# Optimization experiments

Hardware: AMD Instinct MI355X
Metric: run time of the kernel (lower is better)

Reference implementation:

```python
import jax, jax.numpy as jnp
import numpy as np

N_MAX = 5000  # original module truncates both clouds to 5000 points


def _hungarian(cost):
    """Exact linear sum assignment (Jonker-Volgenant / Hungarian with potentials).
    cost: (n, n) float64 numpy array. Returns cols: cols[i] = column assigned to row i.
    Matches scipy.optimize.linear_sum_assignment on square matrices."""
    n = cost.shape[0]
    u = np.zeros(n + 1)
    v = np.zeros(n + 1)
    p = np.full(n + 1, -1, dtype=np.int64)  # p[j] = row matched to column j (-1 = free); col n is virtual
    way = np.zeros(n, dtype=np.int64)
    for i in range(n):
        p[n] = i
        j0 = n
        minv = np.full(n, np.inf)
        used = np.zeros(n + 1, dtype=bool)
        # Dijkstra-style shortest augmenting path, inner step vectorized over columns
        while p[j0] != -1:
            used[j0] = True
            i0 = p[j0]
            free = ~used[:n]
            cur = cost[i0] - u[i0] - v[:n]
            upd = free & (cur < minv)
            minv = np.where(upd, cur, minv)
            way = np.where(upd, j0, way)
            masked = np.where(free, minv, np.inf)
            j1 = int(np.argmin(masked))
            delta = masked[j1]
            used_idx = np.nonzero(used)[0]
            u[p[used_idx]] += delta
            v[used_idx] -= delta
            minv = np.where(free, minv - delta, minv)
            j0 = j1
        # augment along alternating path back to the virtual column
        while j0 != n:
            j1 = way[j0]
            p[j0] = p[j1]
            j0 = int(j1)
    cols = np.empty(n, dtype=np.int64)
    cols[p[:n]] = np.arange(n)
    return cols


def _pairwise_dist(a, b):
    # Euclidean cdist: (n,3) x (m,3) -> (n,m)
    d2 = (jnp.sum(a * a, axis=1)[:, None]
          + jnp.sum(b * b, axis=1)[None, :]
          - 2.0 * (a @ b.T))
    return jnp.sqrt(jnp.maximum(d2, 0.0))


def setup_inputs() -> dict:
    key = jax.random.key(0)
    k1, k2 = jax.random.split(key)
    gt_pc = jax.random.normal(k1, (1, 1024, 3), dtype=jnp.float32)
    gen_pc = jax.random.normal(k2, (1, 1024, 3), dtype=jnp.float32)
    return {"gt_pc": gt_pc, "gen_pc": gen_pc}


def reference(gt_pc, gen_pc):
    # squeeze() + truncate to 5000 points, as in the torch module
    a = gt_pc.reshape(-1, gt_pc.shape[-1])[:N_MAX]
    b = gen_pc.reshape(-1, gen_pc.shape[-1])[:N_MAX]
    d = _pairwise_dist(a, b)  # (n, n) full cost matrix
    # exact optimal assignment (host-side, data dependent -> not jittable)
    cols = _hungarian(np.asarray(d, dtype=np.float64))
    rows = jnp.arange(d.shape[0])
    return d[rows, jnp.asarray(cols)].mean()
```

## Files before the change

kernel.cpp:

```cpp
#include <hip/hip_runtime.h>
#include <math.h>


#define N         1024
#define NT        512
#define NW        (NT / 64)
#define CPL       16
#define NPHASE    3
#define ROUND_CAP 30000

typedef unsigned long long ull;

__device__ __forceinline__ float wave_min_bcast(float x) {
#define DPPSTEP(C) { int _t = __builtin_amdgcn_update_dpp(                    \
      __float_as_int(x), __float_as_int(x), (C), 0xf, 0xf, false);            \
      x = fminf(x, __int_as_float(_t)); }
    DPPSTEP(0x111)
    DPPSTEP(0x112)
    DPPSTEP(0x114)
    DPPSTEP(0x118)
    DPPSTEP(0x142)
    DPPSTEP(0x143)
#undef DPPSTEP
    return __int_as_float(__builtin_amdgcn_readlane(__float_as_int(x), 63));
}

__device__ __forceinline__ float dist_b(const float4 Ai, float bxn, float byn,
                                        float bzn, float sbk) {
    float acc = fmaf(bzn, Ai.z, sbk);
    acc = fmaf(byn, Ai.y, acc);
    acc = fmaf(bxn, Ai.x, acc);
    return __builtin_amdgcn_sqrtf(fmaxf(acc + Ai.w, 0.0f));
}

__global__ __launch_bounds__(NT, 1)
void emd_auction(const float* __restrict__ gt, const float* __restrict__ gen,
                 float* __restrict__ out)
{
    __shared__ float4 A[N];
    __shared__ float4 B[N];
    __shared__ float  p[N];
    __shared__ ull    bidPack[N];
    __shared__ int    owner[N];
    __shared__ int    pobj[N];
    __shared__ int    freeBuf[2][N];
    __shared__ int    bidList[N];
    __shared__ int    bidFlag[N];
    __shared__ int    s_cnt[2];
    __shared__ int    s_nbid;
    __shared__ double partial[NW];

    const int tid  = threadIdx.x;
    const int lane = tid & 63;
    const int wid  = tid >> 6;

    float bxn[CPL], byn[CPL], bzn[CPL], sb[CPL];
    #pragma unroll
    for (int k = 0; k < CPL; ++k) {
        const int j = (k << 6) | lane;
        const float gx = gen[3*j], gy = gen[3*j+1], gz = gen[3*j+2];
        bxn[k] = -2.f*gx; byn[k] = -2.f*gy; bzn[k] = -2.f*gz;
        sb[k]  = gx*gx + gy*gy + gz*gz;
    }
    for (int i = tid; i < N; i += NT) {
        const float x = gt[3*i], y = gt[3*i+1], z = gt[3*i+2];
        A[i] = make_float4(x, y, z, x*x + y*y + z*z);
        const float gx = gen[3*i], gy = gen[3*i+1], gz = gen[3*i+2];
        B[i] = make_float4(gx, gy, gz, gx*gx + gy*gy + gz*gz);
        p[i] = 0.f; bidPack[i] = 0ull; bidFlag[i] = 0;
        owner[i] = -1; pobj[i] = -1;
    }
    if (tid == 0) s_nbid = 0;
    __syncthreads();

    const float EPS[NPHASE] = {0.25f, 0.033f, 4e-3f};
    int  rounds  = 0;
    bool aborted = false;
    int  cur     = 0;

    for (int ph = 0; ph < NPHASE && !aborted; ++ph) {
        const float eps = EPS[ph];

        if (ph > 0) {
            for (int i = wid; i < N; i += NW) {
                const int j = pobj[i];
                if (j < 0) continue;
                const float4 Ai = A[i];
                float m1 = INFINITY;
                #pragma unroll
                for (int k = 0; k < CPL; ++k) {
                    const int jj = (k << 6) | lane;
                    m1 = fminf(m1, dist_b(Ai, bxn[k], byn[k], bzn[k], sb[k])
                                   + p[jj]);
                }
                const float g1 = wave_min_bcast(m1);
                const float4 Bj = B[j];
                const float dot = Ai.x*Bj.x + Ai.y*Bj.y + Ai.z*Bj.z;
                const float rcj = __builtin_amdgcn_sqrtf(
                                      fmaxf(Ai.w + Bj.w - 2.f*dot, 0.f)) + p[j];
                if (rcj > g1 + eps && lane == 0) { owner[j] = -1; pobj[i] = -1; }
            }
            __syncthreads();
        }
        if (tid == 0) { s_cnt[0] = 0; s_cnt[1] = 0; }
        cur = 0;
        __syncthreads();
        for (int base = 0; base < N; base += NT) {
            const int i = base + tid;
            const bool fr = (pobj[i] < 0);
            const ull m = __ballot(fr);
            int pos = 0;
            if (lane == 0 && m) pos = atomicAdd(&s_cnt[0], __popcll(m));
            pos = __shfl(pos, 0);
            if (fr) freeBuf[0][pos + __popcll(m & ((1ull << lane) - 1ull))] = i;
        }
        __syncthreads();

        for (;;) {
            const int nf = s_cnt[cur];
            if (nf == 0) break;
            if (++rounds >= ROUND_CAP) { aborted = true; break; }
            const int nxt = cur ^ 1;
            if (tid == 0) s_cnt[nxt] = 0;

            for (int t = wid; t < nf; t += NW) {
                const int i = freeBuf[cur][t];
                const float4 Ai = A[i];
                float m1 = INFINITY, m2 = INFINITY; int a1 = 0;
                #pragma unroll
                for (int k = 0; k < CPL; ++k) {
                    const int j = (k << 6) | lane;
                    const float rc =
                        dist_b(Ai, bxn[k], byn[k], bzn[k], sb[k]) + p[j];
                    if (rc < m1)      { m2 = m1; m1 = rc; a1 = j; }
                    else if (rc < m2) { m2 = rc; }
                }
                const float g1 = wave_min_bcast(m1);
                const ull  mm  = __ballot(m1 == g1);
                const int  w1  = __ffsll(mm) - 1;
                const int  j1  = __builtin_amdgcn_readlane(a1, w1);
                const float contrib = (lane == w1) ? m2 : m1;
                const float g2 = wave_min_bcast(contrib);
                if (lane == 0) {
                    const float bid = p[j1] + (g2 - g1) + eps;
                    atomicMax(&bidPack[j1],
                              ((ull)(unsigned)__float_as_int(bid) << 32)
                              | (unsigned)i);
                    if (atomicCAS(&bidFlag[j1], 0, 1) == 0) {
                        const int pos = atomicAdd(&s_nbid, 1);
                        bidList[pos] = j1;
                    }
                }
            }
            __syncthreads();

            const int nbid = s_nbid;
            for (int t = tid; t < nbid; t += NT) {
                const int j  = bidList[t];
                const ull pk = bidPack[j];
                bidPack[j] = 0ull; bidFlag[j] = 0;
                p[j] = __int_as_float((int)(pk >> 32));
                const int inew = (int)(pk & 0xffffffffu);
                const int iold = owner[j];
                owner[j] = inew;
                pobj[inew] = j;
                if (iold >= 0) {
                    pobj[iold] = -1;
                    const int pos = atomicAdd(&s_cnt[nxt], 1);
                    freeBuf[nxt][pos] = iold;
                }
            }
            __syncthreads();

            if (tid == 0) s_nbid = 0;
            for (int base = 0; base < nf; base += NT) {
                const int t = base + tid;
                bool fr = false; int i = 0;
                if (t < nf) { i = freeBuf[cur][t]; fr = (pobj[i] < 0); }
                const ull m = __ballot(fr);
                int pos = 0;
                if (lane == 0 && m) pos = atomicAdd(&s_cnt[nxt], __popcll(m));
                pos = __shfl(pos, 0);
                if (fr)
                    freeBuf[nxt][pos + __popcll(m & ((1ull << lane) - 1ull))] = i;
            }
            __syncthreads();
            cur = nxt;
        }
    }

    {
        const int leftover = s_cnt[cur];
        if (leftover > 0) {
            if (wid == 0) {
                for (int t = 0; t < leftover; ++t) {
                    const int i = freeBuf[cur][t];
                    const float4 Ai = A[i];
                    float m1 = INFINITY; int a1 = 0;
                    #pragma unroll
                    for (int k = 0; k < CPL; ++k) {
                        const int j = (k << 6) | lane;
                        const bool fre = (owner[j] < 0);
                        const float c = dist_b(Ai, bxn[k], byn[k], bzn[k], sb[k]);
                        const float sel = fre ? c : INFINITY;
                        if (sel < m1) { m1 = sel; a1 = j; }
                    }
                    const float g1 = wave_min_bcast(m1);
                    const ull  mm  = __ballot(m1 == g1);
                    const int  w1  = __ffsll(mm) - 1;
                    const int  j1  = __builtin_amdgcn_readlane(a1, w1);
                    if (lane == 0) owner[j1] = i;
                    asm volatile("s_waitcnt lgkmcnt(0)" ::: "memory");
                }
            }
            __syncthreads();
        }
    }

    double s = 0.0;
    for (int j = tid; j < N; j += NT) {
        const int i = owner[j];
        if (i >= 0) {
            const float4 Ai = A[i];
            const float4 Bj = B[j];
            const float dot = Ai.x*Bj.x + Ai.y*Bj.y + Ai.z*Bj.z;
            const float d2  = Ai.w + Bj.w - 2.0f*dot;
            s += (double)__builtin_amdgcn_sqrtf(fmaxf(d2, 0.0f));
        }
    }
    #pragma unroll
    for (int m = 32; m >= 1; m >>= 1) s += __shfl_xor(s, m);
    if (lane == 0) partial[wid] = s;
    __syncthreads();
    if (tid == 0) {
        double tot = 0.0;
        for (int w = 0; w < NW; ++w) tot += partial[w];
        out[0] = (float)(tot / (double)N);
    }
}

extern "C" void kernel_launch(void* const* d_in, const int* in_sizes, int n_in,
                              void* d_out, int out_size, void* d_ws, size_t ws_size,
                              hipStream_t stream) {
    const float* gt  = (const float*)d_in[0];
    const float* gen = (const float*)d_in[1];
    float* out = (float*)d_out;
    emd_auction<<<1, NT, 0, stream>>>(gt, gen, out);
}
```

Baseline: 10.74 ms.

## Warm-start auction prices from column minima and drop free-list compaction

```diff
diff --git a/kernel.cpp b/kernel.cpp
--- a/kernel.cpp
+++ b/kernel.cpp
@@ -7,7 +7,8 @@
 #define NW        (NT / 64)
 #define CPL       16
 #define NPHASE    3
-#define ROUND_CAP 30000
+#define ROUND_CAP 20000
+#define OFFSET    4.0f
 
 typedef unsigned long long ull;
 
@@ -25,12 +26,16 @@
     return __int_as_float(__builtin_amdgcn_readlane(__float_as_int(x), 63));
 }
 
-__device__ __forceinline__ float dist_b(const float4 Ai, float bxn, float byn,
-                                        float bzn, float sbk) {
+__device__ __forceinline__ float dist2_b(const float4 Ai, float bxn, float byn,
+                                         float bzn, float sbk) {
     float acc = fmaf(bzn, Ai.z, sbk);
     acc = fmaf(byn, Ai.y, acc);
     acc = fmaf(bxn, Ai.x, acc);
-    return __builtin_amdgcn_sqrtf(fmaxf(acc + Ai.w, 0.0f));
+    return fmaxf(acc + Ai.w, 0.0f);
+}
+__device__ __forceinline__ float dist_b(const float4 Ai, float bxn, float byn,
+                                        float bzn, float sbk) {
+    return __builtin_amdgcn_sqrtf(dist2_b(Ai, bxn, byn, bzn, sbk));
 }
 
 __global__ __launch_bounds__(NT, 1)
@@ -41,18 +46,17 @@
     __shared__ float4 B[N];
     __shared__ float  p[N];
     __shared__ ull    bidPack[N];
+    __shared__ int    bidList[N];
+    __shared__ int    bidFlag[N];
     __shared__ int    owner[N];
     __shared__ int    pobj[N];
-    __shared__ int    freeBuf[2][N];
-    __shared__ int    bidList[N];
-    __shared__ int    bidFlag[N];
-    __shared__ int    s_cnt[2];
-    __shared__ int    s_nbid;
+    __shared__ int    s_nbid, s_nfree;
     __shared__ double partial[NW];
 
     const int tid  = threadIdx.x;
     const int lane = tid & 63;
     const int wid  = tid >> 6;
+    unsigned* pu = (unsigned*)p;
 
     float bxn[CPL], byn[CPL], bzn[CPL], sb[CPL];
     #pragma unroll
@@ -67,88 +71,109 @@
         A[i] = make_float4(x, y, z, x*x + y*y + z*z);
         const float gx = gen[3*i], gy = gen[3*i+1], gz = gen[3*i+2];
         B[i] = make_float4(gx, gy, gz, gx*gx + gy*gy + gz*gz);
-        p[i] = 0.f; bidPack[i] = 0ull; bidFlag[i] = 0;
+        pu[i] = 0x7F800000u;
+        bidPack[i] = 0ull; bidFlag[i] = 0;
         owner[i] = -1; pobj[i] = -1;
     }
-    if (tid == 0) s_nbid = 0;
+    if (tid == 0) { s_nbid = 0; s_nfree = N; }
     __syncthreads();
 
-    const float EPS[NPHASE] = {0.25f, 0.033f, 4e-3f};
+    {
+        float rmin[CPL];
+        #pragma unroll
+        for (int k = 0; k < CPL; ++k) rmin[k] = INFINITY;
+        for (int r = 0; r < N / NW; ++r) {
+            const float4 Ai = A[wid * (N / NW) + r];
+            #pragma unroll
+            for (int k = 0; k < CPL; ++k)
+                rmin[k] = fminf(rmin[k],
+                                dist2_b(Ai, bxn[k], byn[k], bzn[k], sb[k]));
+        }
+        #pragma unroll
+        for (int k = 0; k < CPL; ++k)
+            atomicMin(&pu[(k << 6) | lane], (unsigned)__float_as_int(rmin[k]));
+        __syncthreads();
+        for (int j = tid; j < N; j += NT)
+            p[j] = OFFSET - __builtin_amdgcn_sqrtf(p[j]);
+        __syncthreads();
+    }
+
+    const float EPS[NPHASE] = {0.1f, 0.02f, 4e-3f};
     int  rounds  = 0;
     bool aborted = false;
-    int  cur     = 0;
 
     for (int ph = 0; ph < NPHASE && !aborted; ++ph) {
         const float eps = EPS[ph];
 
         if (ph > 0) {
-            for (int i = wid; i < N; i += NW) {
-                const int j = pobj[i];
-                if (j < 0) continue;
-                const float4 Ai = A[i];
-                float m1 = INFINITY;
-                #pragma unroll
-                for (int k = 0; k < CPL; ++k) {
-                    const int jj = (k << 6) | lane;
-                    m1 = fminf(m1, dist_b(Ai, bxn[k], byn[k], bzn[k], sb[k])
-                                   + p[jj]);
+            if (tid == 0) s_nfree = 0;
+            for (int c = 0; c < 2; ++c) {
+                const int i = (((wid << 1) | c) << 6) | lane;
+                ull mask = __ballot(pobj[i] >= 0);
+                while (mask) {
+                    const int l = __ffsll(mask) - 1; mask &= mask - 1;
+                    const int person = (((wid << 1) | c) << 6) | l;
+                    const int j = pobj[person];
+                    const float4 Ai = A[person];
+                    float m1 = INFINITY;
+                    #pragma unroll
+                    for (int k = 0; k < CPL; ++k) {
+                        const int jj = (k << 6) | lane;
+                        m1 = fminf(m1,
+                            dist_b(Ai, bxn[k], byn[k], bzn[k], sb[k]) + p[jj]);
+                    }
+                    const float g1 = wave_min_bcast(m1);
+                    if (lane == 0) {
+                        const float4 Bj = B[j];
+                        const float dot = Ai.x*Bj.x + Ai.y*Bj.y + Ai.z*Bj.z;
+                        const float rcj = __builtin_amdgcn_sqrtf(
+                            fmaxf(Ai.w + Bj.w - 2.f*dot, 0.f)) + p[j];
+                        if (rcj > g1 + eps) { owner[j] = -1; pobj[person] = -1; }
+                    }
                 }
-                const float g1 = wave_min_bcast(m1);
-                const float4 Bj = B[j];
-                const float dot = Ai.x*Bj.x + Ai.y*Bj.y + Ai.z*Bj.z;
-                const float rcj = __builtin_amdgcn_sqrtf(
-                                      fmaxf(Ai.w + Bj.w - 2.f*dot, 0.f)) + p[j];
-                if (rcj > g1 + eps && lane == 0) { owner[j] = -1; pobj[i] = -1; }
-            }
-            __syncthreads();
-        }
-        if (tid == 0) { s_cnt[0] = 0; s_cnt[1] = 0; }
-        cur = 0;
-        __syncthreads();
-        for (int base = 0; base < N; base += NT) {
-            const int i = base + tid;
-            const bool fr = (pobj[i] < 0);
-            const ull m = __ballot(fr);
-            int pos = 0;
-            if (lane == 0 && m) pos = atomicAdd(&s_cnt[0], __popcll(m));
-            pos = __shfl(pos, 0);
-            if (fr) freeBuf[0][pos + __popcll(m & ((1ull << lane) - 1ull))] = i;
-        }
-        __syncthreads();
+            }
+            __syncthreads();
+            for (int c = 0; c < 2; ++c) {
+                const int i = (((wid << 1) | c) << 6) | lane;
+                const ull m = __ballot(pobj[i] < 0);
+                if (lane == 0 && m) atomicAdd(&s_nfree, __popcll(m));
+            }
+            __syncthreads();
+        }
 
         for (;;) {
-            const int nf = s_cnt[cur];
+            const int nf = s_nfree;
             if (nf == 0) break;
             if (++rounds >= ROUND_CAP) { aborted = true; break; }
-            const int nxt = cur ^ 1;
-            if (tid == 0) s_cnt[nxt] = 0;
-
-            for (int t = wid; t < nf; t += NW) {
-                const int i = freeBuf[cur][t];
-                const float4 Ai = A[i];
-                float m1 = INFINITY, m2 = INFINITY; int a1 = 0;
-                #pragma unroll
-                for (int k = 0; k < CPL; ++k) {
-                    const int j = (k << 6) | lane;
-                    const float rc =
-                        dist_b(Ai, bxn[k], byn[k], bzn[k], sb[k]) + p[j];
-                    if (rc < m1)      { m2 = m1; m1 = rc; a1 = j; }
-                    else if (rc < m2) { m2 = rc; }
-                }
-                const float g1 = wave_min_bcast(m1);
-                const ull  mm  = __ballot(m1 == g1);
-                const int  w1  = __ffsll(mm) - 1;
-                const int  j1  = __builtin_amdgcn_readlane(a1, w1);
-                const float contrib = (lane == w1) ? m2 : m1;
-                const float g2 = wave_min_bcast(contrib);
-                if (lane == 0) {
-                    const float bid = p[j1] + (g2 - g1) + eps;
-                    atomicMax(&bidPack[j1],
-                              ((ull)(unsigned)__float_as_int(bid) << 32)
-                              | (unsigned)i);
-                    if (atomicCAS(&bidFlag[j1], 0, 1) == 0) {
-                        const int pos = atomicAdd(&s_nbid, 1);
-                        bidList[pos] = j1;
+
+            for (int c = 0; c < 2; ++c) {
+                const int i = (((wid << 1) | c) << 6) | lane;
+                ull mask = __ballot(pobj[i] < 0);
+                while (mask) {
+                    const int l = __ffsll(mask) - 1; mask &= mask - 1;
+                    const int person = (((wid << 1) | c) << 6) | l;
+                    const float4 Ai = A[person];
+                    float m1 = INFINITY, m2 = INFINITY, c1 = 0.f; int a1 = 0;
+                    #pragma unroll
+                    for (int k = 0; k < CPL; ++k) {
+                        const int jj = (k << 6) | lane;
+                        const float c0 = dist_b(Ai, bxn[k], byn[k], bzn[k], sb[k]);
+                        const float rc = c0 + p[jj];
+                        if (rc < m1)      { m2 = m1; m1 = rc; a1 = jj; c1 = c0; }
+                        else if (rc < m2) { m2 = rc; }
+                    }
+                    const float g1 = wave_min_bcast(m1);
+                    const ull  bm  = __ballot(m1 == g1);
+                    const int  w1  = __ffsll(bm) - 1;
+                    const float contrib = (lane == w1) ? m2 : m1;
+                    const float g2 = wave_min_bcast(contrib);
+                    if (lane == w1) {
+                        const float bid = (g2 - c1) + eps;
+                        atomicMax(&bidPack[a1],
+                                  ((ull)(unsigned)__float_as_int(bid) << 32)
+                                  | (unsigned)person);
+                        if (atomicCAS(&bidFlag[a1], 0, 1) == 0)
+                            bidList[atomicAdd(&s_nbid, 1)] = a1;
                     }
                 }
             }
@@ -164,57 +189,37 @@
                 const int iold = owner[j];
                 owner[j] = inew;
                 pobj[inew] = j;
-                if (iold >= 0) {
-                    pobj[iold] = -1;
-                    const int pos = atomicAdd(&s_cnt[nxt], 1);
-                    freeBuf[nxt][pos] = iold;
+                if (iold >= 0) pobj[iold] = -1;
+                else atomicSub(&s_nfree, 1);
+            }
+            if (tid == 0) s_nbid = 0;
+            __syncthreads();
+        }
+    }
+
+    if (aborted) {
+        if (wid == 0) {
+            for (int i = 0; i < N; ++i) {
+                if (pobj[i] >= 0) continue;
+                const float4 Ai = A[i];
+                float m1 = INFINITY; int a1 = 0;
+                #pragma unroll
+                for (int k = 0; k < CPL; ++k) {
+                    const int jj = (k << 6) | lane;
+                    const bool fre = (owner[jj] < 0);
+                    const float c = dist_b(Ai, bxn[k], byn[k], bzn[k], sb[k]);
+                    const float sel = fre ? c : INFINITY;
+                    if (sel < m1) { m1 = sel; a1 = jj; }
                 }
-            }
-            __syncthreads();
-
-            if (tid == 0) s_nbid = 0;
-            for (int base = 0; base < nf; base += NT) {
-                const int t = base + tid;
-                bool fr = false; int i = 0;
-                if (t < nf) { i = freeBuf[cur][t]; fr = (pobj[i] < 0); }
-                const ull m = __ballot(fr);
-                int pos = 0;
-                if (lane == 0 && m) pos = atomicAdd(&s_cnt[nxt], __popcll(m));
-                pos = __shfl(pos, 0);
-                if (fr)
-                    freeBuf[nxt][pos + __popcll(m & ((1ull << lane) - 1ull))] = i;
-            }
-            __syncthreads();
-            cur = nxt;
-        }
-    }
-
-    {
-        const int leftover = s_cnt[cur];
-        if (leftover > 0) {
-            if (wid == 0) {
-                for (int t = 0; t < leftover; ++t) {
-                    const int i = freeBuf[cur][t];
-                    const float4 Ai = A[i];
-                    float m1 = INFINITY; int a1 = 0;
-                    #pragma unroll
-                    for (int k = 0; k < CPL; ++k) {
-                        const int j = (k << 6) | lane;
-                        const bool fre = (owner[j] < 0);
-                        const float c = dist_b(Ai, bxn[k], byn[k], bzn[k], sb[k]);
-                        const float sel = fre ? c : INFINITY;
-                        if (sel < m1) { m1 = sel; a1 = j; }
-                    }
-                    const float g1 = wave_min_bcast(m1);
-                    const ull  mm  = __ballot(m1 == g1);
-                    const int  w1  = __ffsll(mm) - 1;
-                    const int  j1  = __builtin_amdgcn_readlane(a1, w1);
-                    if (lane == 0) owner[j1] = i;
-                    asm volatile("s_waitcnt lgkmcnt(0)" ::: "memory");
-                }
-            }
-            __syncthreads();
-        }
+                const float g1 = wave_min_bcast(m1);
+                const ull  bm  = __ballot(m1 == g1);
+                const int  w1  = __ffsll(bm) - 1;
+                const int  j1  = __builtin_amdgcn_readlane(a1, w1);
+                if (lane == 0) { owner[j1] = i; pobj[i] = j1; }
+                asm volatile("s_waitcnt lgkmcnt(0)" ::: "memory");
+            }
+        }
+        __syncthreads();
     }
 
     double s = 0.0;
```

Measured after the change: 8.813 ms. 1.22x faster.
